# Performance work log

Measured on AMD Instinct MI355X. Metric: run time of the kernel, lower is better.

## Reference

```python
import jax, jax.numpy as jnp
import numpy as np

D = 128          # input_dim
H = 512          # hidden_dim = max(64, 4*D)
C = 10           # n_classes
T = 15           # n_trees
DEPTH = 3        # tree_depth
I = 2 ** DEPTH - 1   # n_internal = 7
L = 2 ** DEPTH       # n_leaves = 8
PPT = I * (D + 1) + L * C   # params_per_tree = 983
P = T * PPT                  # total_params = 14745
LN_EPS = 1e-5
B_TRAIN = 100000
B_TEST = 100000


def setup_inputs() -> dict:
    key = jax.random.key(0)
    ks = jax.random.split(key, 16)
    s = 0.02
    return {
        "X_train": jax.random.normal(ks[0], (B_TRAIN, D), jnp.float32),
        "X_test": jax.random.normal(ks[1], (B_TEST, D), jnp.float32),
        "enc_W1": jax.random.normal(ks[2], (H, D), jnp.float32) * s,
        "enc_b1": jnp.zeros((H,), jnp.float32),
        "ln1_g": jnp.ones((H,), jnp.float32),
        "ln1_b": jnp.zeros((H,), jnp.float32),
        "enc_W2": jax.random.normal(ks[3], (H, H), jnp.float32) * s,
        "enc_b2": jnp.zeros((H,), jnp.float32),
        "ln2_g": jnp.ones((H,), jnp.float32),
        "ln2_b": jnp.zeros((H,), jnp.float32),
        "head_W1": jax.random.normal(ks[4], (C, H, H), jnp.float32) * s,
        "head_b1": jnp.zeros((C, H), jnp.float32),
        "head_W2": jax.random.normal(ks[5], (C, P, H), jnp.float32) * s,
        "head_b2": jax.random.normal(ks[6], (C, P), jnp.float32) * s,
        "tree_weights": jnp.ones((T,), jnp.float32) / T,
    }


def _layernorm(x, g, b):
    m = x.mean(-1, keepdims=True)
    v = ((x - m) ** 2).mean(-1, keepdims=True)
    return (x - m) * jax.lax.rsqrt(v + LN_EPS) * g + b


def reference(X_train, X_test, enc_W1, enc_b1, ln1_g, ln1_b, enc_W2, enc_b2,
              ln2_g, ln2_b, head_W1, head_b1, head_W2, head_b2, tree_weights):
    # data encoder on the train-mean vector (dropout is identity in eval)
    mean = X_train.mean(0)                                  # [D]
    h = jax.nn.relu(_layernorm(enc_W1 @ mean + enc_b1, ln1_g, ln1_b))
    h = jax.nn.relu(_layernorm(enc_W2 @ h + enc_b2, ln2_g, ln2_b))   # [H]

    # all class heads at once: params [C, P]
    hh = jax.nn.relu(jnp.einsum('chd,d->ch', head_W1, h) + head_b1)
    params = jnp.einsum('cph,ch->cp', head_W2, hh) + head_b2

    # unpack per-tree params: [C, T, ...]
    p = params.reshape(C, T, PPT)
    split_w = p[..., :I * D].reshape(C, T, I, D)
    split_b = p[..., I * D:I * D + I]                       # [C, T, I]
    leaf_logits = p[..., I * D + I:].reshape(C, T, L, C)

    # soft routing (only the first DEPTH internal nodes are used, as in the source)
    routes = jax.nn.sigmoid(
        jnp.einsum('bd,ctid->ctbi', X_test, split_w) + split_b[:, :, None, :]
    )                                                       # [C, T, B, I]
    lp = jnp.ones(routes.shape[:3] + (1,), routes.dtype)    # [C, T, B, 1]
    for d in range(DEPTH):
        left = routes[..., d:d + 1]
        lp = jnp.concatenate([lp * left, lp * (1.0 - left)], axis=-1)
    # lp: [C, T, B, L]

    tree_out = jax.nn.softmax(leaf_logits, axis=-1)         # [C, T, L, C]
    probs = jnp.einsum('ctbl,ctlk->ctbk', lp[..., :L], tree_out)
    w = jax.nn.softmax(tree_weights)                        # [T]
    ens = jnp.einsum('t,ctbk->cbk', w, probs)               # per-head ensemble
    return ens.mean(0)                                      # [B, C]
```

## Files before the change

### kernel.cpp

```cpp
#include <hip/hip_runtime.h>

#define DD 128
#define NC 10
#define NT 15
#define NCT 150
#define NCOLS 450
#define BTRAIN 100000
#define BTEST 100000
#define GROWS 70050
#define NGRP 38

typedef __attribute__((ext_vector_type(8))) __bf16 bf16x8;
typedef __attribute__((ext_vector_type(4))) float f32x4;
typedef __attribute__((ext_vector_type(8))) unsigned short u16x8;

static __device__ __forceinline__ unsigned short f2bf(float f) {
  unsigned int u = __builtin_bit_cast(unsigned int, f);
  u = (u + 0x7FFFu + ((u >> 16) & 1u)) >> 16;
  return (unsigned short)u;
}

__global__ void __launch_bounds__(256) k_colsum(const float* __restrict__ X, float* __restrict__ partial) {
  int tid = threadIdx.x;
  int gid = blockIdx.x * 256 + tid;
  int stride = gridDim.x * 256;
  float sx = 0.f, sy = 0.f, sz = 0.f, sw = 0.f;
  const float4* Xv = (const float4*)X;
  for (int i = gid; i < BTRAIN * 32; i += stride) {
    float4 v = Xv[i];
    sx += v.x; sy += v.y; sz += v.z; sw += v.w;
  }
  __shared__ float red[256][4];
  red[tid][0] = sx; red[tid][1] = sy; red[tid][2] = sz; red[tid][3] = sw;
  __syncthreads();
  for (int off = 128; off >= 32; off >>= 1) {
    if (tid < off) {
      red[tid][0] += red[tid + off][0];
      red[tid][1] += red[tid + off][1];
      red[tid][2] += red[tid + off][2];
      red[tid][3] += red[tid + off][3];
    }
    __syncthreads();
  }
  if (tid < 32) {
#pragma unroll
    for (int i = 0; i < 4; ++i)
      partial[blockIdx.x * 128 + tid * 4 + i] = red[tid][i];
  }
}

__global__ void __launch_bounds__(512) k_enc1(const float* __restrict__ partial, const float* __restrict__ W1,
                                              const float* __restrict__ b1, const float* __restrict__ g,
                                              const float* __restrict__ bb, float* __restrict__ out) {
  __shared__ float mS[DD];
  __shared__ float red[512];
  int t = threadIdx.x;
  {
    int c = t & 127, qd = t >> 7;
    float s = 0.0f;
    const float* pp = partial + (size_t)qd * 128 * 128 + c;
    for (int k = 0; k < 128; ++k) s += pp[k * 128];
    red[t] = s; __syncthreads();
    if (t < 128) mS[t] = (red[t] + red[t + 128] + red[t + 256] + red[t + 384]) * (1.0f / BTRAIN);
    __syncthreads();
  }
  float z = b1[t];
  const float4* w = (const float4*)(W1 + t * DD);
#pragma unroll
  for (int j = 0; j < DD / 4; ++j) {
    float4 wv = w[j];
    z += wv.x * mS[4 * j] + wv.y * mS[4 * j + 1] + wv.z * mS[4 * j + 2] + wv.w * mS[4 * j + 3];
  }
  __syncthreads();
  red[t] = z; __syncthreads();
  for (int off = 256; off > 0; off >>= 1) { if (t < off) red[t] += red[t + off]; __syncthreads(); }
  float m = red[0] * (1.0f / 512.0f); __syncthreads();
  float d = z - m;
  red[t] = d * d; __syncthreads();
  for (int off = 256; off > 0; off >>= 1) { if (t < off) red[t] += red[t + off]; __syncthreads(); }
  float v = red[0] * (1.0f / 512.0f);
  out[t] = fmaxf(d * rsqrtf(v + 1e-5f) * g[t] + bb[t], 0.0f);
}

template <int RELU>
__global__ void __launch_bounds__(256) k_matvec512(const float* __restrict__ W, const float* __restrict__ x,
                                                   const float* __restrict__ bias, float* __restrict__ out, int rows) {
  int wv = threadIdx.x >> 6, lane = threadIdx.x & 63;
  int row = blockIdx.x * 4 + wv;
  if (row >= rows) return;
  const float4* wr = (const float4*)(W + (size_t)row * 512) + lane * 2;
  const float4* xv = (const float4*)x + lane * 2;
  float4 a0 = wr[0], a1 = wr[1], x0 = xv[0], x1 = xv[1];
  float s = a0.x * x0.x + a0.y * x0.y + a0.z * x0.z + a0.w * x0.w
          + a1.x * x1.x + a1.y * x1.y + a1.z * x1.z + a1.w * x1.w;
#pragma unroll
  for (int off = 32; off > 0; off >>= 1) s += __shfl_down(s, off);
  if (lane == 0) {
    s += bias[row];
    if (RELU) s = fmaxf(s, 0.0f);
    out[row] = s;
  }
}

__global__ void __launch_bounds__(512) k_ln(const float* __restrict__ z, const float* __restrict__ g,
                                            const float* __restrict__ bb, float* __restrict__ out) {
  __shared__ float red[512];
  int t = threadIdx.x;
  float zv = z[t];
  red[t] = zv; __syncthreads();
  for (int off = 256; off > 0; off >>= 1) { if (t < off) red[t] += red[t + off]; __syncthreads(); }
  float m = red[0] * (1.0f / 512.0f); __syncthreads();
  float d = zv - m;
  red[t] = d * d; __syncthreads();
  for (int off = 256; off > 0; off >>= 1) { if (t < off) red[t] += red[t + off]; __syncthreads(); }
  float v = red[0] * (1.0f / 512.0f);
  out[t] = fmaxf(d * rsqrtf(v + 1e-5f) * g[t] + bb[t], 0.0f);
}

__global__ void __launch_bounds__(256) k_params(const float* __restrict__ W2, const float* __restrict__ hh,
                                                const float* __restrict__ b2, unsigned short* __restrict__ Wb,
                                                float* __restrict__ sb, float* __restrict__ leaf) {
  int wv = threadIdx.x >> 6, lane = threadIdx.x & 63;
  int base = (blockIdx.x * 4 + wv) * 8;
  if (base >= GROWS) return;
  float4 a[8][2];
  size_t rowoff[8];
  int ctArr[8], wArr[8], cArr[8];
#pragma unroll
  for (int i = 0; i < 8; ++i) {
    int R = base + i;
    if (R >= GROWS) R = GROWS - 1;
    int ctIdx = R / 467;
    int w = R - ctIdx * 467;
    int c = ctIdx / 15;
    int t = ctIdx - c * 15;
    int p;
    if (w < 384) p = t * 983 + w;
    else if (w < 387) p = t * 983 + 896 + (w - 384);
    else p = t * 983 + 903 + (w - 387);
    rowoff[i] = (size_t)c * 14745 + p;
    ctArr[i] = ctIdx; wArr[i] = w; cArr[i] = c;
    const float4* wr = (const float4*)(W2 + rowoff[i] * 512) + lane * 2;
    a[i][0] = wr[0];
    a[i][1] = wr[1];
  }
#pragma unroll
  for (int i = 0; i < 8; ++i) {
    const float4* xv = (const float4*)(hh + cArr[i] * 512) + lane * 2;
    float4 x0 = xv[0], x1 = xv[1];
    float s = a[i][0].x * x0.x + a[i][0].y * x0.y + a[i][0].z * x0.z + a[i][0].w * x0.w
            + a[i][1].x * x1.x + a[i][1].y * x1.y + a[i][1].z * x1.z + a[i][1].w * x1.w;
#pragma unroll
    for (int off = 32; off > 0; off >>= 1) s += __shfl_down(s, off);
    if (lane == 0) {
      s += b2[rowoff[i]];
      int w = wArr[i], ctIdx = ctArr[i];
      if (w < 384) {
        int ii = w >> 7, d = w & 127;
        Wb[(size_t)(ctIdx * 3 + ii) * DD + d] = f2bf(s);
      } else if (w < 387) {
        sb[ctIdx * 3 + (w - 384)] = s;
      } else {
        leaf[ctIdx * 80 + (w - 387)] = s;
      }
    }
  }
}

__global__ void k_tob(const float* __restrict__ leaf, const float* __restrict__ tw, unsigned short* __restrict__ TOB) {
  int g = blockIdx.x;
  int lane = threadIdx.x;
  int ct = g * 4 + (lane >> 4);
  int cls = lane & 15;
  float mx = tw[0];
  for (int i = 1; i < 15; ++i) mx = fmaxf(mx, tw[i]);
  float wsum = 0.0f;
  for (int i = 0; i < 15; ++i) wsum += __expf(tw[i] - mx);
  u16x8 o;
#pragma unroll
  for (int j = 0; j < 8; ++j) {
    float v = 0.0f;
    if (ct < NCT && cls < NC) {
      float wt = __expf(tw[ct % 15] - mx) / wsum;
      const float* lr = leaf + ct * 80 + j * 10;
      float m2 = lr[0];
#pragma unroll
      for (int k = 1; k < 10; ++k) m2 = fmaxf(m2, lr[k]);
      float es = 0.0f;
#pragma unroll
      for (int k = 0; k < 10; ++k) es += __expf(lr[k] - m2);
      v = __expf(lr[cls] - m2) / es * wt * (1.0f / (float)NC);
    }
    o[j] = f2bf(v);
  }
  *(u16x8*)&TOB[((size_t)g * 64 + lane) * 8] = o;
}

__global__ void __launch_bounds__(256) k_fused(const float* __restrict__ X, const unsigned short* __restrict__ Wb,
                                               const float* __restrict__ sb, const unsigned short* __restrict__ TOB,
                                               float* __restrict__ out) {
  __shared__ union {
    unsigned short Xs[64][152];
    _Float16 Rs[64][242];
  } sU;
  int tid = threadIdx.x;
  int b0 = blockIdx.x * 64;
  {
    int row = tid >> 2, seg = tid & 3;
    int gb = b0 + row;
    const float4* xr = (const float4*)(X + (size_t)gb * DD) + seg * 8;
#pragma unroll
    for (int j2 = 0; j2 < 4; ++j2) {
      bf16x8 u;
      if (gb < BTEST) {
        float4 va = xr[2 * j2], vb = xr[2 * j2 + 1];
        u[0] = (__bf16)va.x; u[1] = (__bf16)va.y; u[2] = (__bf16)va.z; u[3] = (__bf16)va.w;
        u[4] = (__bf16)vb.x; u[5] = (__bf16)vb.y; u[6] = (__bf16)vb.z; u[7] = (__bf16)vb.w;
      } else {
#pragma unroll
        for (int j = 0; j < 8; ++j) u[j] = (__bf16)0.0f;
      }
      *(u16x8*)&sU.Xs[row][seg * 32 + j2 * 8] = __builtin_bit_cast(u16x8, u);
    }
  }
  __syncthreads();
  int wv = tid >> 6, lane = tid & 63;
  int m = lane & 15, g = lane >> 4;
  bf16x8 A[4][4];
#pragma unroll
  for (int rt = 0; rt < 4; ++rt)
#pragma unroll
    for (int ks = 0; ks < 4; ++ks)
      A[rt][ks] = __builtin_bit_cast(bf16x8, *(const u16x8*)&sU.Xs[rt * 16 + m][ks * 32 + g * 8]);
  __syncthreads();
  f32x4 accA = 0.0f, accB = 0.0f;
  int pl = wv * 16 + m;
#pragma unroll
  for (int pass = 0; pass < 2; ++pass) {
    int passBase = pass ? 240 : 0;
    {
      int tstart, tcnt;
      if (pass == 0) { tstart = wv * 4; tcnt = (wv == 3) ? 3 : 4; }
      else { tstart = 15 + ((wv < 2) ? wv * 4 : (8 + (wv - 2) * 3)); tcnt = (wv < 2) ? 4 : 3; }
      int col = tstart * 16 + m;
      u16x8 Bv[4];
#pragma unroll
      for (int ks = 0; ks < 4; ++ks)
        Bv[ks] = *(const u16x8*)&Wb[(size_t)col * DD + ks * 32 + g * 8];
      float sbv = sb[col];
      for (int it = 0; it < tcnt; ++it) {
        int pc = (it + 1 < tcnt) ? (col + 16) : col;
        u16x8 Bn[4];
#pragma unroll
        for (int ks = 0; ks < 4; ++ks)
          Bn[ks] = *(const u16x8*)&Wb[(size_t)pc * DD + ks * 32 + g * 8];
        float sbn = sb[pc];
        f32x4 acc[4];
#pragma unroll
        for (int rt = 0; rt < 4; ++rt) acc[rt] = 0.0f;
#pragma unroll
        for (int ks = 0; ks < 4; ++ks) {
          bf16x8 Bf = __builtin_bit_cast(bf16x8, Bv[ks]);
#pragma unroll
          for (int rt = 0; rt < 4; ++rt)
            acc[rt] = __builtin_amdgcn_mfma_f32_16x16x32_bf16(A[rt][ks], Bf, acc[rt], 0, 0, 0);
        }
        int colLocal = col - passBase;
#pragma unroll
        for (int rt = 0; rt < 4; ++rt)
#pragma unroll
          for (int r = 0; r < 4; ++r) {
            float pre = acc[rt][r] + sbv;
            float e = __expf(-pre);
            float sg = __builtin_amdgcn_rcpf(1.0f + e);
            sU.Rs[rt * 16 + g * 4 + r][colLocal] = (_Float16)sg;
          }
#pragma unroll
        for (int ks = 0; ks < 4; ++ks) Bv[ks] = Bn[ks];
        sbv = sbn;
        col += 16;
      }
    }
    __syncthreads();
    {
      int gbase = pass ? 20 : 0;
      int gn = pass ? 18 : 20;
      int ctl = g;
      for (int gi = 0; gi < gn; ++gi) {
        int gAbs = gbase + gi;
        int ct = gAbs * 4 + ctl;
        int cb = 3 * ct - passBase;
        float l0 = (float)sU.Rs[pl][cb + 0];
        float l1 = (float)sU.Rs[pl][cb + 1];
        float l2 = (float)sU.Rs[pl][cb + 2];
        float n0 = 1.0f - l0, n1 = 1.0f - l1, n2 = 1.0f - l2;
        float p00 = l1 * l0, p01 = l1 * n0, p10 = n1 * l0, p11 = n1 * n0;
        bf16x8 av;
        av[0] = (__bf16)(l2 * p00); av[1] = (__bf16)(l2 * p01);
        av[2] = (__bf16)(l2 * p10); av[3] = (__bf16)(l2 * p11);
        av[4] = (__bf16)(n2 * p00); av[5] = (__bf16)(n2 * p01);
        av[6] = (__bf16)(n2 * p10); av[7] = (__bf16)(n2 * p11);
        u16x8 bv = *(const u16x8*)&TOB[((size_t)gAbs * 64 + lane) * 8];
        if (gi & 1)
          accB = __builtin_amdgcn_mfma_f32_16x16x32_bf16(av, __builtin_bit_cast(bf16x8, bv), accB, 0, 0, 0);
        else
          accA = __builtin_amdgcn_mfma_f32_16x16x32_bf16(av, __builtin_bit_cast(bf16x8, bv), accA, 0, 0, 0);
      }
    }
    __syncthreads();
  }
  f32x4 accT = accA + accB;
  int cls = lane & 15;
  if (cls < NC) {
#pragma unroll
    for (int r = 0; r < 4; ++r) {
      int b = b0 + wv * 16 + (lane >> 4) * 4 + r;
      if (b < BTEST) out[(size_t)b * 10 + cls] = accT[r];
    }
  }
}

extern "C" void kernel_launch(void* const* d_in, const int* in_sizes, int n_in,
                              void* d_out, int out_size, void* d_ws, size_t ws_size,
                              hipStream_t stream) {
  const float* Xtr = (const float*)d_in[0];
  const float* Xte = (const float*)d_in[1];
  const float* eW1 = (const float*)d_in[2];
  const float* eb1 = (const float*)d_in[3];
  const float* g1  = (const float*)d_in[4];
  const float* bb1 = (const float*)d_in[5];
  const float* eW2 = (const float*)d_in[6];
  const float* eb2 = (const float*)d_in[7];
  const float* g2  = (const float*)d_in[8];
  const float* bb2 = (const float*)d_in[9];
  const float* hW1 = (const float*)d_in[10];
  const float* hb1 = (const float*)d_in[11];
  const float* hW2 = (const float*)d_in[12];
  const float* hb2 = (const float*)d_in[13];
  const float* tw  = (const float*)d_in[14];

  char* ws = (char*)d_ws;
  const size_t OFF_PART = 0;
  const size_t OFF_H1   = 262144;
  const size_t OFF_Z2   = 264192;
  const size_t OFF_H2   = 266240;
  const size_t OFF_HH   = 268288;
  const size_t OFF_LEAF = 288768;
  const size_t OFF_SB   = 336896;
  const size_t OFF_WB   = 338944;
  const size_t OFF_TOB  = 457728;
  const size_t NEED     = 496640;
  if (ws_size < NEED) return;

  float* partial = (float*)(ws + OFF_PART);
  float* h1 = (float*)(ws + OFF_H1);
  float* z2 = (float*)(ws + OFF_Z2);
  float* h2 = (float*)(ws + OFF_H2);
  float* hhp = (float*)(ws + OFF_HH);
  float* leafp = (float*)(ws + OFF_LEAF);
  float* sbp = (float*)(ws + OFF_SB);
  unsigned short* Wb = (unsigned short*)(ws + OFF_WB);
  unsigned short* TOBp = (unsigned short*)(ws + OFF_TOB);

  k_colsum<<<512, 256, 0, stream>>>(Xtr, partial);
  k_enc1<<<1, 512, 0, stream>>>(partial, eW1, eb1, g1, bb1, h1);
  k_matvec512<0><<<128, 256, 0, stream>>>(eW2, h1, eb2, z2, 512);
  k_ln<<<1, 512, 0, stream>>>(z2, g2, bb2, h2);
  k_matvec512<1><<<1280, 256, 0, stream>>>(hW1, h2, hb1, hhp, 5120);
  k_params<<<2190, 256, 0, stream>>>(hW2, hhp, hb2, Wb, sbp, leafp);
  k_tob<<<NGRP, 64, 0, stream>>>(leafp, tw, TOBp);
  k_fused<<<1563, 256, 0, stream>>>(Xte, Wb, sbp, TOBp, (float*)d_out);
}
```

Measured before the change: 133.7 us.

## Fuse encoder stages into two kernels with redundant per-block LayerNorm

Replaces the four small encoder kernels (enc1, matvec, ln, matvec) with two kernels. Each block recomputes the column mean, the first layer and LN1 itself, then does its slice of the W2 matvec. The head kernel likewise recomputes LN2 per block before its hW1 rows. This removes two launches and the single-block serialization points, at the cost of redundant work: every block rereads the partial sums and W1.

```diff
diff --git a/kernel.cpp b/kernel.cpp
--- a/kernel.cpp
+++ b/kernel.cpp
@@ -49,72 +49,103 @@
   }
 }
 
-__global__ void __launch_bounds__(512) k_enc1(const float* __restrict__ partial, const float* __restrict__ W1,
-                                              const float* __restrict__ b1, const float* __restrict__ g,
-                                              const float* __restrict__ bb, float* __restrict__ out) {
-  __shared__ float mS[DD];
-  __shared__ float red[512];
-  int t = threadIdx.x;
-  {
-    int c = t & 127, qd = t >> 7;
+__global__ void __launch_bounds__(256) k_z2(const float* __restrict__ partial,
+                                            const float* __restrict__ W1, const float* __restrict__ b1,
+                                            const float* __restrict__ g1, const float* __restrict__ bb1,
+                                            const float* __restrict__ W2, const float* __restrict__ b2,
+                                            float* __restrict__ z2g) {
+  __shared__ float mS[128];
+  __shared__ float redS[256];
+  __shared__ float z1S[512];
+  __shared__ float h1S[512];
+  int tid = threadIdx.x;
+  {
+    int c = tid & 127, h = tid >> 7;
     float s = 0.0f;
-    const float* pp = partial + (size_t)qd * 128 * 128 + c;
-    for (int k = 0; k < 128; ++k) s += pp[k * 128];
-    red[t] = s; __syncthreads();
-    if (t < 128) mS[t] = (red[t] + red[t + 128] + red[t + 256] + red[t + 384]) * (1.0f / BTRAIN);
-    __syncthreads();
-  }
-  float z = b1[t];
-  const float4* w = (const float4*)(W1 + t * DD);
-#pragma unroll
-  for (int j = 0; j < DD / 4; ++j) {
-    float4 wv = w[j];
-    z += wv.x * mS[4 * j] + wv.y * mS[4 * j + 1] + wv.z * mS[4 * j + 2] + wv.w * mS[4 * j + 3];
-  }
-  __syncthreads();
-  red[t] = z; __syncthreads();
-  for (int off = 256; off > 0; off >>= 1) { if (t < off) red[t] += red[t + off]; __syncthreads(); }
-  float m = red[0] * (1.0f / 512.0f); __syncthreads();
-  float d = z - m;
-  red[t] = d * d; __syncthreads();
-  for (int off = 256; off > 0; off >>= 1) { if (t < off) red[t] += red[t + off]; __syncthreads(); }
-  float v = red[0] * (1.0f / 512.0f);
-  out[t] = fmaxf(d * rsqrtf(v + 1e-5f) * g[t] + bb[t], 0.0f);
-}
-
-template <int RELU>
-__global__ void __launch_bounds__(256) k_matvec512(const float* __restrict__ W, const float* __restrict__ x,
-                                                   const float* __restrict__ bias, float* __restrict__ out, int rows) {
-  int wv = threadIdx.x >> 6, lane = threadIdx.x & 63;
-  int row = blockIdx.x * 4 + wv;
-  if (row >= rows) return;
-  const float4* wr = (const float4*)(W + (size_t)row * 512) + lane * 2;
-  const float4* xv = (const float4*)x + lane * 2;
-  float4 a0 = wr[0], a1 = wr[1], x0 = xv[0], x1 = xv[1];
-  float s = a0.x * x0.x + a0.y * x0.y + a0.z * x0.z + a0.w * x0.w
-          + a1.x * x1.x + a1.y * x1.y + a1.z * x1.z + a1.w * x1.w;
-#pragma unroll
-  for (int off = 32; off > 0; off >>= 1) s += __shfl_down(s, off);
-  if (lane == 0) {
-    s += bias[row];
-    if (RELU) s = fmaxf(s, 0.0f);
-    out[row] = s;
-  }
-}
-
-__global__ void __launch_bounds__(512) k_ln(const float* __restrict__ z, const float* __restrict__ g,
-                                            const float* __restrict__ bb, float* __restrict__ out) {
-  __shared__ float red[512];
-  int t = threadIdx.x;
-  float zv = z[t];
-  red[t] = zv; __syncthreads();
-  for (int off = 256; off > 0; off >>= 1) { if (t < off) red[t] += red[t + off]; __syncthreads(); }
-  float m = red[0] * (1.0f / 512.0f); __syncthreads();
-  float d = zv - m;
-  red[t] = d * d; __syncthreads();
-  for (int off = 256; off > 0; off >>= 1) { if (t < off) red[t] += red[t + off]; __syncthreads(); }
-  float v = red[0] * (1.0f / 512.0f);
-  out[t] = fmaxf(d * rsqrtf(v + 1e-5f) * g[t] + bb[t], 0.0f);
+    const float* pp = partial + (size_t)(h * 256) * 128 + c;
+    for (int k = 0; k < 256; ++k) s += pp[k * 128];
+    redS[tid] = s;
+    __syncthreads();
+    if (tid < 128) mS[tid] = (redS[tid] + redS[tid + 128]) * (1.0f / BTRAIN);
+    __syncthreads();
+  }
+  for (int r = tid; r < 512; r += 256) {
+    const float4* w = (const float4*)(W1 + (size_t)r * DD);
+    float z = b1[r];
+#pragma unroll
+    for (int j = 0; j < 32; ++j) {
+      float4 wv = w[j];
+      z += wv.x * mS[4 * j] + wv.y * mS[4 * j + 1] + wv.z * mS[4 * j + 2] + wv.w * mS[4 * j + 3];
+    }
+    z1S[r] = z;
+  }
+  __syncthreads();
+  {
+    float a = z1S[tid], b = z1S[tid + 256];
+    redS[tid] = a + b; __syncthreads();
+    for (int off = 128; off > 0; off >>= 1) { if (tid < off) redS[tid] += redS[tid + off]; __syncthreads(); }
+    float m = redS[0] * (1.0f / 512.0f); __syncthreads();
+    float da = a - m, db = b - m;
+    redS[tid] = da * da + db * db; __syncthreads();
+    for (int off = 128; off > 0; off >>= 1) { if (tid < off) redS[tid] += redS[tid + off]; __syncthreads(); }
+    float rs = rsqrtf(redS[0] * (1.0f / 512.0f) + 1e-5f); __syncthreads();
+    h1S[tid] = fmaxf(da * rs * g1[tid] + bb1[tid], 0.0f);
+    h1S[tid + 256] = fmaxf(db * rs * g1[tid + 256] + bb1[tid + 256], 0.0f);
+  }
+  __syncthreads();
+  {
+    int wv = tid >> 6, lane = tid & 63;
+    int r = blockIdx.x * 4 + wv;
+    const float4* wr = (const float4*)(W2 + (size_t)r * 512) + lane * 2;
+    const float4* xv = (const float4*)h1S + lane * 2;
+    float4 a0 = wr[0], a1 = wr[1], x0 = xv[0], x1 = xv[1];
+    float s = a0.x * x0.x + a0.y * x0.y + a0.z * x0.z + a0.w * x0.w
+            + a1.x * x1.x + a1.y * x1.y + a1.z * x1.z + a1.w * x1.w;
+#pragma unroll
+    for (int off = 32; off > 0; off >>= 1) s += __shfl_down(s, off);
+    if (lane == 0) z2g[r] = s + b2[r];
+  }
+}
+
+__global__ void __launch_bounds__(256) k_hh(const float* __restrict__ z2g,
+                                            const float* __restrict__ g2, const float* __restrict__ bb2,
+                                            const float* __restrict__ hW1, const float* __restrict__ hb1,
+                                            float* __restrict__ hh) {
+  __shared__ float redS[256];
+  __shared__ float h2S[512];
+  int tid = threadIdx.x;
+  {
+    float a = z2g[tid], b = z2g[tid + 256];
+    redS[tid] = a + b; __syncthreads();
+    for (int off = 128; off > 0; off >>= 1) { if (tid < off) redS[tid] += redS[tid + off]; __syncthreads(); }
+    float m = redS[0] * (1.0f / 512.0f); __syncthreads();
+    float da = a - m, db = b - m;
+    redS[tid] = da * da + db * db; __syncthreads();
+    for (int off = 128; off > 0; off >>= 1) { if (tid < off) redS[tid] += redS[tid + off]; __syncthreads(); }
+    float rs = rsqrtf(redS[0] * (1.0f / 512.0f) + 1e-5f); __syncthreads();
+    h2S[tid] = fmaxf(da * rs * g2[tid] + bb2[tid], 0.0f);
+    h2S[tid + 256] = fmaxf(db * rs * g2[tid + 256] + bb2[tid + 256], 0.0f);
+  }
+  __syncthreads();
+  int wv = tid >> 6, lane = tid & 63;
+  const float4* xv = (const float4*)h2S + lane * 2;
+  float4 x0 = xv[0], x1 = xv[1];
+  float4 a[4][2];
+  int r0 = blockIdx.x * 16 + wv * 4;
+#pragma unroll
+  for (int i = 0; i < 4; ++i) {
+    const float4* wr = (const float4*)(hW1 + (size_t)(r0 + i) * 512) + lane * 2;
+    a[i][0] = wr[0];
+    a[i][1] = wr[1];
+  }
+#pragma unroll
+  for (int i = 0; i < 4; ++i) {
+    float s = a[i][0].x * x0.x + a[i][0].y * x0.y + a[i][0].z * x0.z + a[i][0].w * x0.w
+            + a[i][1].x * x1.x + a[i][1].y * x1.y + a[i][1].z * x1.z + a[i][1].w * x1.w;
+#pragma unroll
+    for (int off = 32; off > 0; off >>= 1) s += __shfl_down(s, off);
+    if (lane == 0) hh[r0 + i] = fmaxf(s + hb1[r0 + i], 0.0f);
+  }
 }
 
 __global__ void __launch_bounds__(256) k_params(const float* __restrict__ W2, const float* __restrict__ hh,
@@ -341,21 +372,17 @@
 
   char* ws = (char*)d_ws;
   const size_t OFF_PART = 0;
-  const size_t OFF_H1   = 262144;
-  const size_t OFF_Z2   = 264192;
-  const size_t OFF_H2   = 266240;
-  const size_t OFF_HH   = 268288;
-  const size_t OFF_LEAF = 288768;
-  const size_t OFF_SB   = 336896;
-  const size_t OFF_WB   = 338944;
-  const size_t OFF_TOB  = 457728;
-  const size_t NEED     = 496640;
+  const size_t OFF_Z2   = 262144;
+  const size_t OFF_HH   = 264192;
+  const size_t OFF_LEAF = 284672;
+  const size_t OFF_SB   = 332672;
+  const size_t OFF_WB   = 334528;
+  const size_t OFF_TOB  = 453312;
+  const size_t NEED     = 492224;
   if (ws_size < NEED) return;
 
   float* partial = (float*)(ws + OFF_PART);
-  float* h1 = (float*)(ws + OFF_H1);
-  float* z2 = (float*)(ws + OFF_Z2);
-  float* h2 = (float*)(ws + OFF_H2);
+  float* z2p = (float*)(ws + OFF_Z2);
   float* hhp = (float*)(ws + OFF_HH);
   float* leafp = (float*)(ws + OFF_LEAF);
   float* sbp = (float*)(ws + OFF_SB);
@@ -363,10 +390,8 @@
   unsigned short* TOBp = (unsigned short*)(ws + OFF_TOB);
 
   k_colsum<<<512, 256, 0, stream>>>(Xtr, partial);
-  k_enc1<<<1, 512, 0, stream>>>(partial, eW1, eb1, g1, bb1, h1);
-  k_matvec512<0><<<128, 256, 0, stream>>>(eW2, h1, eb2, z2, 512);
-  k_ln<<<1, 512, 0, stream>>>(z2, g2, bb2, h2);
-  k_matvec512<1><<<1280, 256, 0, stream>>>(hW1, h2, hb1, hhp, 5120);
+  k_z2<<<128, 256, 0, stream>>>(partial, eW1, eb1, g1, bb1, eW2, eb2, z2p);
+  k_hh<<<320, 256, 0, stream>>>(z2p, g2, bb2, hW1, hb1, hhp);
   k_params<<<2190, 256, 0, stream>>>(hW2, hhp, hb2, Wb, sbp, leafp);
   k_tob<<<NGRP, 64, 0, stream>>>(leafp, tw, TOBp);
   k_fused<<<1563, 256, 0, stream>>>(Xte, Wb, sbp, TOBp, (float*)d_out);
```

Result: faster. 130.2 us (-2.7%).
